# Kernel optimization log

Hardware: AMD Instinct MI355X
Metric: run time of the kernel (lower is better)

Reference implementation:

```python
import jax, jax.numpy as jnp
import numpy as np

B, S, D, NH, FF = 2, 2048, 1024, 16, 4096
HD = D // NH
SCALE = HD ** -0.5
EPS = 1e-5


def layer_norm(x, g, b):
    mu = jnp.mean(x, axis=-1, keepdims=True)
    var = jnp.var(x, axis=-1, keepdims=True)
    return (x - mu) * jax.lax.rsqrt(var + EPS) * g + b


def setup_inputs() -> dict:
    key = jax.random.key(0)
    ks = jax.random.split(key, 12)
    w = 0.02
    return {
        "x": jax.random.normal(ks[0], (B, S, D), dtype=jnp.float32),
        "ln1_g": jnp.ones((D,), jnp.float32),
        "ln1_b": jnp.zeros((D,), jnp.float32),
        "wq": jax.random.normal(ks[1], (D, D), jnp.float32) * w,
        "wkv": jax.random.normal(ks[2], (D, 2 * D), jnp.float32) * w,
        "wo": jax.random.normal(ks[3], (D, D), jnp.float32) * w,
        "bo": jnp.zeros((D,), jnp.float32),
        "ln2_g": jnp.ones((D,), jnp.float32),
        "ln2_b": jnp.zeros((D,), jnp.float32),
        "w1": jax.random.normal(ks[4], (D, FF), jnp.float32) * w,
        "b1": jnp.zeros((FF,), jnp.float32),
        "w2": jax.random.normal(ks[5], (FF, D), jnp.float32) * w,
        "b2": jnp.zeros((D,), jnp.float32),
    }


def reference(x, ln1_g, ln1_b, wq, wkv, wo, bo, ln2_g, ln2_b, w1, b1, w2, b2):
    # pre-norm self-attention (y=None -> keys = normalized queries), no mask
    h = layer_norm(x, ln1_g, ln1_b)                      # [B,S,D]
    q = (h @ wq).reshape(B, S, NH, HD)                   # [B,S,H,hd]
    kv = (h @ wkv).reshape(B, S, 2, NH, HD)
    k, v = kv[:, :, 0], kv[:, :, 1]                      # [B,S,H,hd]
    scores = jnp.einsum("bnhd,bmhd->bnmh", q, k) * SCALE  # [B,S,S,H]
    attn = jax.nn.softmax(scores, axis=2)
    o = jnp.einsum("bnmh,bmhd->bnhd", attn, v).reshape(B, S, D)
    o = o @ wo + bo
    x = x + o
    h2 = layer_norm(x, ln2_g, ln2_b)
    ff = jnp.maximum(h2 @ w1 + b1, 0.0) @ w2 + b2        # relu MLP, dropout p=0
    return (x + ff, attn)
```

## Files before the change

kernel.cpp:

```cpp
#include <hip/hip_runtime.h>
#include <hip/hip_bf16.h>


constexpr int Bc = 2, Sc = 2048, Dc = 1024, NHc = 16, FFc = 4096;
constexpr int Mrows = Bc * Sc;
constexpr float SCALE_ = 0.125f;
constexpr float EPSc = 1e-5f;
constexpr float L2E = 1.4426950408889634f;
constexpr float SC_L2E = SCALE_ * L2E;

typedef __attribute__((ext_vector_type(8))) short short8;
typedef __attribute__((ext_vector_type(4))) short short4v;
typedef __attribute__((ext_vector_type(4))) float floatx4;

#define DEV static __device__ __forceinline__

DEV short f2b(float f) {
  union { float f; unsigned u; } v; v.f = f;
  unsigned r = v.u + 0x7FFFu + ((v.u >> 16) & 1u);
  return (short)(r >> 16);
}

DEV floatx4 mfma16(short8 a, short8 b, floatx4 c) {
  return __builtin_amdgcn_mfma_f32_16x16x32_bf16(a, b, c, 0, 0, 0);
}

DEV void load_lds16(const short* g, short* l) {
  __builtin_amdgcn_global_load_lds(
      (const __attribute__((address_space(1))) void*)g,
      (__attribute__((address_space(3))) void*)l, 16, 0, 0);
}

__global__ __launch_bounds__(256) void cast_transpose_k(
    const float* __restrict__ W, short* __restrict__ Wt, int K, int N) {
  __shared__ float t[32][33];
  int n0 = blockIdx.x * 32, k0 = blockIdx.y * 32;
  int tx = threadIdx.x & 31, ty = threadIdx.x >> 5;
  for (int r = ty; r < 32; r += 8)
    t[r][tx] = W[(size_t)(k0 + r) * N + n0 + tx];
  __syncthreads();
  for (int r = ty; r < 32; r += 8)
    Wt[(size_t)(n0 + r) * K + k0 + tx] = f2b(t[tx][r]);
}

__global__ __launch_bounds__(256) void layernorm_k(
    const float* __restrict__ x, const float* __restrict__ g,
    const float* __restrict__ bb, short* __restrict__ out) {
  int row = blockIdx.x;
  float4 v = ((const float4*)(x + (size_t)row * Dc))[threadIdx.x];
  float s = v.x + v.y + v.z + v.w;
  float s2 = v.x * v.x + v.y * v.y + v.z * v.z + v.w * v.w;
#pragma unroll
  for (int off = 32; off >= 1; off >>= 1) {
    s += __shfl_xor(s, off);
    s2 += __shfl_xor(s2, off);
  }
  __shared__ float red[8];
  int wave = threadIdx.x >> 6, lane = threadIdx.x & 63;
  if (lane == 0) { red[wave] = s; red[4 + wave] = s2; }
  __syncthreads();
  s = red[0] + red[1] + red[2] + red[3];
  s2 = red[4] + red[5] + red[6] + red[7];
  float mu = s * (1.0f / Dc);
  float var = s2 * (1.0f / Dc) - mu * mu;
  float rstd = rsqrtf(var + EPSc);
  int c = threadIdx.x * 4;
  float4 gv = ((const float4*)g)[threadIdx.x];
  float4 bv = ((const float4*)bb)[threadIdx.x];
  short4v o;
  o.x = f2b((v.x - mu) * rstd * gv.x + bv.x);
  o.y = f2b((v.y - mu) * rstd * gv.y + bv.y);
  o.z = f2b((v.z - mu) * rstd * gv.z + bv.z);
  o.w = f2b((v.w - mu) * rstd * gv.w + bv.w);
  *(short4v*)(out + (size_t)row * Dc + c) = o;
}

template <int OUTF>
__global__ __launch_bounds__(256) void gemm_bt_k(
    const short* __restrict__ A, const short* __restrict__ Bt,
    const float* __restrict__ bias, const float* __restrict__ resid,
    void* __restrict__ Cout, int M, int N, int K, int relu) {
  __shared__ short As[128 * 32];
  __shared__ short Bs[128 * 32];
  int tid = threadIdx.x;
  int wave = tid >> 6, lane = tid & 63, quad = lane >> 4, l16 = lane & 15;
  int m0 = blockIdx.y * 128, n0 = blockIdx.x * 128;
  int wm = (wave & 1) * 64, wn = (wave >> 1) * 64;
  int lrow = lane >> 2, lcol = (lane & 3) * 8;
  const short* Ab0 = A + (size_t)(m0 + wave * 32 + lrow) * K + lcol;
  const short* Ab1 = A + (size_t)(m0 + wave * 32 + 16 + lrow) * K + lcol;
  const short* Bb0 = Bt + (size_t)(n0 + wave * 32 + lrow) * K + lcol;
  const short* Bb1 = Bt + (size_t)(n0 + wave * 32 + 16 + lrow) * K + lcol;
  short* Al0 = &As[(wave * 2 + 0) * 512];
  short* Al1 = &As[(wave * 2 + 1) * 512];
  short* Bl0 = &Bs[(wave * 2 + 0) * 512];
  short* Bl1 = &Bs[(wave * 2 + 1) * 512];
  floatx4 acc[4][4] = {};
  for (int k0 = 0; k0 < K; k0 += 32) {
    __syncthreads();
    load_lds16(Ab0 + k0, Al0);
    load_lds16(Ab1 + k0, Al1);
    load_lds16(Bb0 + k0, Bl0);
    load_lds16(Bb1 + k0, Bl1);
    __syncthreads();
    short8 af[4], bf[4];
#pragma unroll
    for (int i = 0; i < 4; ++i)
      af[i] = *(const short8*)(&As[(wm + i * 16 + l16) * 32 + quad * 8]);
#pragma unroll
    for (int j = 0; j < 4; ++j)
      bf[j] = *(const short8*)(&Bs[(wn + j * 16 + l16) * 32 + quad * 8]);
#pragma unroll
    for (int i = 0; i < 4; ++i)
#pragma unroll
      for (int j = 0; j < 4; ++j)
        acc[i][j] = mfma16(af[i], bf[j], acc[i][j]);
  }
#pragma unroll
  for (int i = 0; i < 4; ++i) {
    int row = m0 + wm + i * 16 + quad * 4;
#pragma unroll
    for (int j = 0; j < 4; ++j) {
      int col = n0 + wn + j * 16 + l16;
      float bv = bias ? bias[col] : 0.0f;
#pragma unroll
      for (int r = 0; r < 4; ++r) {
        float v = acc[i][j][r] + bv;
        if (resid) v += resid[(size_t)(row + r) * N + col];
        if (relu) v = fmaxf(v, 0.0f);
        if (OUTF == 0)
          ((short*)Cout)[(size_t)(row + r) * N + col] = f2b(v);
        else
          ((float*)Cout)[(size_t)(row + r) * N + col] = v;
      }
    }
  }
}

__global__ __launch_bounds__(256) void transpose_v_k(
    const short* __restrict__ kv, short* __restrict__ vT) {
  __shared__ short t[64][65];
  int bh = blockIdx.y, b = bh >> 4, h = bh & 15;
  int m0 = blockIdx.x * 64;
  int c = threadIdx.x & 63, ty = threadIdx.x >> 6;
  for (int r = ty; r < 64; r += 4)
    t[r][c] = kv[(size_t)(b * Sc + m0 + r) * 2048 + 1024 + h * 64 + c];
  __syncthreads();
  for (int dd = ty; dd < 64; dd += 4)
    vT[((size_t)bh * 64 + dd) * Sc + m0 + c] = t[c][dd];
}

__global__ __launch_bounds__(256) void attn_stats_k(
    const short* __restrict__ q, const short* __restrict__ kv,
    float* __restrict__ m_i, float* __restrict__ inv_l) {
  int bh = blockIdx.y, b = bh >> 4, h = bh & 15;
  int wave = threadIdx.x >> 6, lane = threadIdx.x & 63, quad = lane >> 4,
      l16 = lane & 15;
  int n0 = blockIdx.x * 64 + wave * 16;
  const short* qp = q + (size_t)(b * Sc + n0 + l16) * Dc + h * 64 + quad * 8;
  short8 qf0 = *(const short8*)qp;
  short8 qf1 = *(const short8*)(qp + 32);
  const short* kb = kv + (size_t)b * Sc * 2048 + h * 64 + quad * 8;
  float rm[4], rl[4];
#pragma unroll
  for (int r = 0; r < 4; ++r) { rm[r] = -1e30f; rl[r] = 0.0f; }
  for (int m0 = 0; m0 < Sc; m0 += 16) {
    const short* kp = kb + (size_t)(m0 + l16) * 2048;
    short8 kf0 = *(const short8*)kp;
    short8 kf1 = *(const short8*)(kp + 32);
    floatx4 s = {0.0f, 0.0f, 0.0f, 0.0f};
    s = mfma16(qf0, kf0, s);
    s = mfma16(qf1, kf1, s);
#pragma unroll
    for (int r = 0; r < 4; ++r) {
      float sv = s[r] * SC_L2E;
      if (sv <= rm[r]) {
        rl[r] += exp2f(sv - rm[r]);
      } else {
        rl[r] = rl[r] * exp2f(rm[r] - sv) + 1.0f;
        rm[r] = sv;
      }
    }
  }
#pragma unroll
  for (int off = 1; off < 16; off <<= 1) {
#pragma unroll
    for (int r = 0; r < 4; ++r) {
      float om = __shfl_xor(rm[r], off);
      float ol = __shfl_xor(rl[r], off);
      float nm = fmaxf(rm[r], om);
      rl[r] = rl[r] * exp2f(rm[r] - nm) + ol * exp2f(om - nm);
      rm[r] = nm;
    }
  }
  if (l16 == 0) {
    int n = n0 + quad * 4;
#pragma unroll
    for (int r = 0; r < 4; ++r) {
      m_i[(size_t)bh * Sc + n + r] = rm[r];
      inv_l[(size_t)bh * Sc + n + r] = 1.0f / rl[r];
    }
  }
}

__global__ __launch_bounds__(256) void attn_write_k(
    const short* __restrict__ q, const short* __restrict__ kv,
    const float* __restrict__ m_i, const float* __restrict__ inv_l,
    float* __restrict__ attn) {
  constexpr int HP = 20;
  __shared__ float P[32 * 16 * HP];
  __shared__ float sm[16][32], sl[16][32];
  int b = blockIdx.z;
  int n0 = blockIdx.y * 32, m0 = blockIdx.x * 16;
  int tid = threadIdx.x;
  int wave = tid >> 6, lane = tid & 63, quad = lane >> 4, l16 = lane & 15;
  for (int i = tid; i < 512; i += 256) {
    int h = i >> 5, nn = i & 31;
    sm[h][nn] = m_i[(size_t)(b * 16 + h) * Sc + n0 + nn];
    sl[h][nn] = inv_l[(size_t)(b * 16 + h) * Sc + n0 + nn];
  }
  __syncthreads();
#pragma unroll
  for (int hh = 0; hh < 4; ++hh) {
    int h = wave * 4 + hh;
    const short* kp = kv + (size_t)(b * Sc + m0 + l16) * 2048 + h * 64 + quad * 8;
    short8 kf0 = *(const short8*)kp;
    short8 kf1 = *(const short8*)(kp + 32);
#pragma unroll
    for (int ni = 0; ni < 2; ++ni) {
      const short* qp =
          q + (size_t)(b * Sc + n0 + ni * 16 + l16) * Dc + h * 64 + quad * 8;
      short8 qf0 = *(const short8*)qp;
      short8 qf1 = *(const short8*)(qp + 32);
      floatx4 s = {0.0f, 0.0f, 0.0f, 0.0f};
      s = mfma16(qf0, kf0, s);
      s = mfma16(qf1, kf1, s);
#pragma unroll
      for (int r = 0; r < 4; ++r) {
        int nn = ni * 16 + quad * 4 + r;
        float p = exp2f(s[r] * SC_L2E - sm[h][nn]) * sl[h][nn];
        P[(nn * 16 + l16) * HP + h] = p;
      }
    }
  }
  __syncthreads();
  size_t base = ((size_t)(b * Sc + n0) * Sc + m0) * 16;
  int w = tid >> 6, l = tid & 63;
  int ml = l >> 2, h4 = (l & 3) * 4;
  for (int n = w; n < 32; n += 4) {
    float4 v = *(const float4*)&P[(n * 16 + ml) * HP + h4];
    *(float4*)&attn[base + (size_t)n * (Sc * 16) + ml * 16 + h4] = v;
  }
}

__global__ __launch_bounds__(256) void attn_pv_k(
    const short* __restrict__ q, const short* __restrict__ kv,
    const short* __restrict__ vT, const float* __restrict__ m_i,
    const float* __restrict__ inv_l, short* __restrict__ o) {
  constexpr int PPAD = 40;
  __shared__ short P[4][16 * PPAD];
  int bh = blockIdx.y, b = bh >> 4, h = bh & 15;
  int wave = threadIdx.x >> 6, lane = threadIdx.x & 63, quad = lane >> 4,
      l16 = lane & 15;
  int n0 = blockIdx.x * 64 + wave * 16;
  const short* qp = q + (size_t)(b * Sc + n0 + l16) * Dc + h * 64 + quad * 8;
  short8 qf0 = *(const short8*)qp;
  short8 qf1 = *(const short8*)(qp + 32);
  float mm[4], il[4];
#pragma unroll
  for (int r = 0; r < 4; ++r) {
    int n = n0 + quad * 4 + r;
    mm[r] = m_i[(size_t)bh * Sc + n];
    il[r] = inv_l[(size_t)bh * Sc + n];
  }
  floatx4 oacc[4] = {};
  const short* kb = kv + (size_t)b * Sc * 2048 + h * 64 + quad * 8;
  const short* vb = vT + (size_t)bh * 64 * Sc;
  short* myP = &P[wave][0];
  for (int m0 = 0; m0 < Sc; m0 += 32) {
#pragma unroll
    for (int ms = 0; ms < 2; ++ms) {
      const short* kp = kb + (size_t)(m0 + ms * 16 + l16) * 2048;
      short8 kf0 = *(const short8*)kp;
      short8 kf1 = *(const short8*)(kp + 32);
      floatx4 s = {0.0f, 0.0f, 0.0f, 0.0f};
      s = mfma16(qf0, kf0, s);
      s = mfma16(qf1, kf1, s);
#pragma unroll
      for (int r = 0; r < 4; ++r) {
        float p = exp2f(s[r] * SC_L2E - mm[r]);
        myP[(quad * 4 + r) * PPAD + ms * 16 + l16] = f2b(p);
      }
    }
    short8 pf = *(const short8*)(&myP[l16 * PPAD + quad * 8]);
#pragma unroll
    for (int ds = 0; ds < 4; ++ds) {
      short8 vf = *(const short8*)(vb + (size_t)(ds * 16 + l16) * Sc + m0 + quad * 8);
      oacc[ds] = mfma16(pf, vf, oacc[ds]);
    }
  }
#pragma unroll
  for (int ds = 0; ds < 4; ++ds)
#pragma unroll
    for (int r = 0; r < 4; ++r)
      o[(size_t)(b * Sc + n0 + quad * 4 + r) * Dc + h * 64 + ds * 16 + l16] =
          f2b(oacc[ds][r] * il[r]);
}

extern "C" void kernel_launch(void* const* d_in, const int* in_sizes, int n_in,
                              void* d_out, int out_size, void* d_ws,
                              size_t ws_size, hipStream_t stream) {
  const float* x = (const float*)d_in[0];
  const float* ln1g = (const float*)d_in[1];
  const float* ln1b = (const float*)d_in[2];
  const float* wq = (const float*)d_in[3];
  const float* wkv = (const float*)d_in[4];
  const float* wo = (const float*)d_in[5];
  const float* bo = (const float*)d_in[6];
  const float* ln2g = (const float*)d_in[7];
  const float* ln2b = (const float*)d_in[8];
  const float* w1 = (const float*)d_in[9];
  const float* b1 = (const float*)d_in[10];
  const float* w2 = (const float*)d_in[11];
  const float* b2 = (const float*)d_in[12];

  char* ws = (char*)d_ws;
  const size_t MB = 1024 * 1024;
  short* wqT  = (short*)(ws + 0 * MB);
  short* wkvT = (short*)(ws + 2 * MB);
  short* woT  = (short*)(ws + 6 * MB);
  short* w1T  = (short*)(ws + 8 * MB);
  short* w2T  = (short*)(ws + 16 * MB);
  short* h    = (short*)(ws + 24 * MB);
  float* x2   = (float*)(ws + 32 * MB);
  float* m_i  = (float*)(ws + 48 * MB);
  float* invl = (float*)(ws + 48 * MB + 256 * 1024);
  short* o    = (short*)(ws + 49 * MB);
  short* qb   = (short*)(ws + 57 * MB);
  short* kvb  = (short*)(ws + 65 * MB);
  short* vT   = (short*)(ws + 81 * MB);
  short* ff1  = (short*)(ws + 57 * MB);

  float* out0 = (float*)d_out;
  float* attn = (float*)d_out + (size_t)Bc * Sc * Dc;

  cast_transpose_k<<<dim3(Dc / 32, Dc / 32), 256, 0, stream>>>(wq, wqT, Dc, Dc);
  cast_transpose_k<<<dim3(2048 / 32, Dc / 32), 256, 0, stream>>>(wkv, wkvT, Dc, 2048);
  cast_transpose_k<<<dim3(Dc / 32, Dc / 32), 256, 0, stream>>>(wo, woT, Dc, Dc);
  cast_transpose_k<<<dim3(FFc / 32, Dc / 32), 256, 0, stream>>>(w1, w1T, Dc, FFc);
  cast_transpose_k<<<dim3(Dc / 32, FFc / 32), 256, 0, stream>>>(w2, w2T, FFc, Dc);

  layernorm_k<<<Mrows, 256, 0, stream>>>(x, ln1g, ln1b, h);

  gemm_bt_k<0><<<dim3(Dc / 128, Mrows / 128), 256, 0, stream>>>(
      h, wqT, nullptr, nullptr, qb, Mrows, Dc, Dc, 0);
  gemm_bt_k<0><<<dim3(2048 / 128, Mrows / 128), 256, 0, stream>>>(
      h, wkvT, nullptr, nullptr, kvb, Mrows, 2048, Dc, 0);

  transpose_v_k<<<dim3(Sc / 64, Bc * NHc), 256, 0, stream>>>(kvb, vT);
  attn_stats_k<<<dim3(Sc / 64, Bc * NHc), 256, 0, stream>>>(qb, kvb, m_i, invl);
  attn_write_k<<<dim3(Sc / 16, Sc / 32, Bc), 256, 0, stream>>>(qb, kvb, m_i, invl, attn);
  attn_pv_k<<<dim3(Sc / 64, Bc * NHc), 256, 0, stream>>>(qb, kvb, vT, m_i, invl, o);

  gemm_bt_k<1><<<dim3(Dc / 128, Mrows / 128), 256, 0, stream>>>(
      o, woT, bo, x, x2, Mrows, Dc, Dc, 0);
  layernorm_k<<<Mrows, 256, 0, stream>>>(x2, ln2g, ln2b, h);
  gemm_bt_k<0><<<dim3(FFc / 128, Mrows / 128), 256, 0, stream>>>(
      h, w1T, b1, nullptr, ff1, Mrows, FFc, Dc, 1);
  gemm_bt_k<1><<<dim3(Dc / 128, Mrows / 128), 256, 0, stream>>>(
      ff1, w2T, b2, x2, out0, Mrows, Dc, FFc, 0);
}
```

Measured before the change: 1.425 ms.

## Fuse attention-probability write with PV product using split-K partial outputs

Merges the kernel that writes normalized attention probabilities with the P·V kernel. Each block now computes QK^T once, writes the fp32 probabilities to the attention output, and accumulates P·V for four heads over a 512-key chunk. The four per-chunk fp32 partial outputs are summed and cast to bf16 in a new reduction kernel. This removes the duplicated QK^T and exp work, but adds a 64MB partial buffer, an extra kernel pass, two block barriers per key step, and a larger register footprint from the 4x4 accumulator array.

```diff
diff --git a/kernel.cpp b/kernel.cpp
--- a/kernel.cpp
+++ b/kernel.cpp
@@ -203,108 +203,106 @@
   }
 }
 
-__global__ __launch_bounds__(256) void attn_write_k(
+__global__ __launch_bounds__(256) void attn_fused_k(
     const short* __restrict__ q, const short* __restrict__ kv,
-    const float* __restrict__ m_i, const float* __restrict__ inv_l,
-    float* __restrict__ attn) {
+    const short* __restrict__ vT, const float* __restrict__ m_i,
+    const float* __restrict__ inv_l, float* __restrict__ attn,
+    float* __restrict__ opart) {
   constexpr int HP = 20;
-  __shared__ float P[32 * 16 * HP];
-  __shared__ float sm[16][32], sl[16][32];
-  int b = blockIdx.z;
-  int n0 = blockIdx.y * 32, m0 = blockIdx.x * 16;
+  __shared__ float P[16 * 32 * HP];
+  __shared__ short pw[4][16 * 40];
+  __shared__ float sm[16][16], sl[16][16];
+  int b = blockIdx.z, mc = blockIdx.x;
+  int n0 = blockIdx.y * 16;
   int tid = threadIdx.x;
   int wave = tid >> 6, lane = tid & 63, quad = lane >> 4, l16 = lane & 15;
-  for (int i = tid; i < 512; i += 256) {
-    int h = i >> 5, nn = i & 31;
+  {
+    int h = tid >> 4, nn = tid & 15;
     sm[h][nn] = m_i[(size_t)(b * 16 + h) * Sc + n0 + nn];
     sl[h][nn] = inv_l[(size_t)(b * 16 + h) * Sc + n0 + nn];
   }
+  short8 qf[4][2];
+#pragma unroll
+  for (int hh = 0; hh < 4; ++hh) {
+    const short* qp =
+        q + (size_t)(b * Sc + n0 + l16) * Dc + (wave * 4 + hh) * 64 + quad * 8;
+    qf[hh][0] = *(const short8*)qp;
+    qf[hh][1] = *(const short8*)(qp + 32);
+  }
+  floatx4 oacc[4][4] = {};
+  short* myP = &pw[wave][0];
   __syncthreads();
-#pragma unroll
-  for (int hh = 0; hh < 4; ++hh) {
-    int h = wave * 4 + hh;
-    const short* kp = kv + (size_t)(b * Sc + m0 + l16) * 2048 + h * 64 + quad * 8;
-    short8 kf0 = *(const short8*)kp;
-    short8 kf1 = *(const short8*)(kp + 32);
-#pragma unroll
-    for (int ni = 0; ni < 2; ++ni) {
-      const short* qp =
-          q + (size_t)(b * Sc + n0 + ni * 16 + l16) * Dc + h * 64 + quad * 8;
-      short8 qf0 = *(const short8*)qp;
-      short8 qf1 = *(const short8*)(qp + 32);
-      floatx4 s = {0.0f, 0.0f, 0.0f, 0.0f};
-      s = mfma16(qf0, kf0, s);
-      s = mfma16(qf1, kf1, s);
-#pragma unroll
-      for (int r = 0; r < 4; ++r) {
-        int nn = ni * 16 + quad * 4 + r;
-        float p = exp2f(s[r] * SC_L2E - sm[h][nn]) * sl[h][nn];
-        P[(nn * 16 + l16) * HP + h] = p;
+  int mend = mc * 512 + 512;
+  for (int m0 = mc * 512; m0 < mend; m0 += 32) {
+#pragma unroll
+    for (int hh = 0; hh < 4; ++hh) {
+      int h = wave * 4 + hh;
+      const short* kb =
+          kv + (size_t)(b * Sc + m0 + l16) * 2048 + h * 64 + quad * 8;
+#pragma unroll
+      for (int ms = 0; ms < 2; ++ms) {
+        const short* kp = kb + (size_t)ms * 16 * 2048;
+        short8 kf0 = *(const short8*)kp;
+        short8 kf1 = *(const short8*)(kp + 32);
+        floatx4 s = {0.0f, 0.0f, 0.0f, 0.0f};
+        s = mfma16(qf[hh][0], kf0, s);
+        s = mfma16(qf[hh][1], kf1, s);
+#pragma unroll
+        for (int r = 0; r < 4; ++r) {
+          int nn = quad * 4 + r;
+          float p = exp2f(s[r] * SC_L2E - sm[h][nn]) * sl[h][nn];
+          P[(nn * 32 + ms * 16 + l16) * HP + h] = p;
+          myP[nn * 40 + ms * 16 + l16] = f2b(p);
+        }
       }
-    }
-  }
-  __syncthreads();
-  size_t base = ((size_t)(b * Sc + n0) * Sc + m0) * 16;
-  int w = tid >> 6, l = tid & 63;
-  int ml = l >> 2, h4 = (l & 3) * 4;
-  for (int n = w; n < 32; n += 4) {
-    float4 v = *(const float4*)&P[(n * 16 + ml) * HP + h4];
-    *(float4*)&attn[base + (size_t)n * (Sc * 16) + ml * 16 + h4] = v;
-  }
-}
-
-__global__ __launch_bounds__(256) void attn_pv_k(
-    const short* __restrict__ q, const short* __restrict__ kv,
-    const short* __restrict__ vT, const float* __restrict__ m_i,
-    const float* __restrict__ inv_l, short* __restrict__ o) {
-  constexpr int PPAD = 40;
-  __shared__ short P[4][16 * PPAD];
-  int bh = blockIdx.y, b = bh >> 4, h = bh & 15;
-  int wave = threadIdx.x >> 6, lane = threadIdx.x & 63, quad = lane >> 4,
-      l16 = lane & 15;
-  int n0 = blockIdx.x * 64 + wave * 16;
-  const short* qp = q + (size_t)(b * Sc + n0 + l16) * Dc + h * 64 + quad * 8;
-  short8 qf0 = *(const short8*)qp;
-  short8 qf1 = *(const short8*)(qp + 32);
-  float mm[4], il[4];
-#pragma unroll
-  for (int r = 0; r < 4; ++r) {
-    int n = n0 + quad * 4 + r;
-    mm[r] = m_i[(size_t)bh * Sc + n];
-    il[r] = inv_l[(size_t)bh * Sc + n];
-  }
-  floatx4 oacc[4] = {};
-  const short* kb = kv + (size_t)b * Sc * 2048 + h * 64 + quad * 8;
-  const short* vb = vT + (size_t)bh * 64 * Sc;
-  short* myP = &P[wave][0];
-  for (int m0 = 0; m0 < Sc; m0 += 32) {
-#pragma unroll
-    for (int ms = 0; ms < 2; ++ms) {
-      const short* kp = kb + (size_t)(m0 + ms * 16 + l16) * 2048;
-      short8 kf0 = *(const short8*)kp;
-      short8 kf1 = *(const short8*)(kp + 32);
-      floatx4 s = {0.0f, 0.0f, 0.0f, 0.0f};
-      s = mfma16(qf0, kf0, s);
-      s = mfma16(qf1, kf1, s);
-#pragma unroll
-      for (int r = 0; r < 4; ++r) {
-        float p = exp2f(s[r] * SC_L2E - mm[r]);
-        myP[(quad * 4 + r) * PPAD + ms * 16 + l16] = f2b(p);
+      short8 pa = *(const short8*)(&myP[l16 * 40 + quad * 8]);
+      const short* vb = vT + ((size_t)(b * 16 + h) * 64) * Sc;
+#pragma unroll
+      for (int dt = 0; dt < 4; ++dt) {
+        short8 vf =
+            *(const short8*)(vb + (size_t)(dt * 16 + l16) * Sc + m0 + quad * 8);
+        oacc[hh][dt] = mfma16(pa, vf, oacc[hh][dt]);
       }
     }
-    short8 pf = *(const short8*)(&myP[l16 * PPAD + quad * 8]);
-#pragma unroll
-    for (int ds = 0; ds < 4; ++ds) {
-      short8 vf = *(const short8*)(vb + (size_t)(ds * 16 + l16) * Sc + m0 + quad * 8);
-      oacc[ds] = mfma16(pf, vf, oacc[ds]);
-    }
-  }
-#pragma unroll
-  for (int ds = 0; ds < 4; ++ds)
-#pragma unroll
-    for (int r = 0; r < 4; ++r)
-      o[(size_t)(b * Sc + n0 + quad * 4 + r) * Dc + h * 64 + ds * 16 + l16] =
-          f2b(oacc[ds][r] * il[r]);
+    __syncthreads();
+    size_t base = (((size_t)b * Sc + n0) * Sc + m0) * 16;
+    for (int t = tid; t < 2048; t += 256) {
+      int nn = t >> 7, rem = t & 127;
+      int ml = rem >> 2, h4 = (rem & 3) * 4;
+      float4 v = *(const float4*)&P[(nn * 32 + ml) * HP + h4];
+      *(float4*)&attn[base + (size_t)nn * (Sc * 16) + ml * 16 + h4] = v;
+    }
+    __syncthreads();
+  }
+  float* op = opart + (size_t)mc * ((size_t)Bc * Sc * Dc) +
+              ((size_t)b * Sc + n0) * Dc;
+#pragma unroll
+  for (int hh = 0; hh < 4; ++hh)
+#pragma unroll
+    for (int dt = 0; dt < 4; ++dt)
+#pragma unroll
+      for (int r = 0; r < 4; ++r)
+        op[(size_t)(quad * 4 + r) * Dc + (wave * 4 + hh) * 64 + dt * 16 + l16] =
+            oacc[hh][dt][r];
+}
+
+__global__ __launch_bounds__(256) void opart_reduce_k(
+    const float* __restrict__ op, short* __restrict__ o) {
+  const size_t PS = (size_t)Bc * Sc * Dc;
+  const size_t n4 = PS / 4;
+  for (size_t i = (size_t)blockIdx.x * 256 + threadIdx.x; i < n4;
+       i += (size_t)gridDim.x * 256) {
+    float4 a = ((const float4*)op)[i];
+    float4 b = ((const float4*)(op + PS))[i];
+    float4 c = ((const float4*)(op + 2 * PS))[i];
+    float4 d = ((const float4*)(op + 3 * PS))[i];
+    short4v s;
+    s.x = f2b(a.x + b.x + c.x + d.x);
+    s.y = f2b(a.y + b.y + c.y + d.y);
+    s.z = f2b(a.z + b.z + c.z + d.z);
+    s.w = f2b(a.w + b.w + c.w + d.w);
+    ((short4v*)o)[i] = s;
+  }
 }
 
 extern "C" void kernel_launch(void* const* d_in, const int* in_sizes, int n_in,
@@ -339,6 +337,7 @@
   short* qb   = (short*)(ws + 57 * MB);
   short* kvb  = (short*)(ws + 65 * MB);
   short* vT   = (short*)(ws + 81 * MB);
+  float* opart= (float*)(ws + 96 * MB);
   short* ff1  = (short*)(ws + 57 * MB);
 
   float* out0 = (float*)d_out;
@@ -359,8 +358,9 @@
 
   transpose_v_k<<<dim3(Sc / 64, Bc * NHc), 256, 0, stream>>>(kvb, vT);
   attn_stats_k<<<dim3(Sc / 64, Bc * NHc), 256, 0, stream>>>(qb, kvb, m_i, invl);
-  attn_write_k<<<dim3(Sc / 16, Sc / 32, Bc), 256, 0, stream>>>(qb, kvb, m_i, invl, attn);
-  attn_pv_k<<<dim3(Sc / 64, Bc * NHc), 256, 0, stream>>>(qb, kvb, vT, m_i, invl, o);
+  attn_fused_k<<<dim3(4, Sc / 16, Bc), 256, 0, stream>>>(
+      qb, kvb, vT, m_i, invl, attn, opart);
+  opart_reduce_k<<<2048, 256, 0, stream>>>(opart, o);
 
   gemm_bt_k<1><<<dim3(Dc / 128, Mrows / 128), 256, 0, stream>>>(
       o, woT, bo, x, x2, Mrows, Dc, Dc, 0);
```

New measurement: 1.279 ms. 1.11x faster.
